# Performance work log

Hardware: AMD Instinct MI355X
Metric: run time of the kernel (lower is better)

## Reference

```python
import jax, jax.numpy as jnp
import numpy as np

B, M, H, NH = 64, 512, 1024, 8
HD = H // NH
EPS = 1e-5


def setup_inputs() -> dict:
    key = jax.random.key(0)
    ks = jax.random.split(key, 16)
    def n(k, shape, s=0.02):
        return jax.random.normal(k, shape, dtype=jnp.float32) * s
    z = lambda shape: jnp.zeros(shape, jnp.float32)
    return {
        "x": jax.random.normal(ks[0], (B, M, M), dtype=jnp.float32),
        # 1x1 Conv2d(1->H): weight [H,1,1,1] flattened to [H], plus bias [H]
        "conv_w": n(ks[1], (H,)), "conv_b": n(ks[2], (H,)),
        # MLP: Linear(M->H), ReLU, Linear(H->H); weights stored [in,out]
        "w1": n(ks[3], (M, H)), "b1": z((H,)),
        "w2": n(ks[4], (H, H)), "b2": z((H,)),
        "ln_g": jnp.ones((H,), jnp.float32), "ln_b": z((H,)),
        "wq": n(ks[5], (H, H)), "bq": z((H,)),
        "wk": n(ks[6], (H, H)), "bk": z((H,)),
        "wv": n(ks[7], (H, H)), "bv": z((H,)),
        "wo": n(ks[8], (H, H)), "bo": z((H,)),
        "wp": n(ks[9], (H, H)), "bp": z((H,)),
    }


def reference(x, conv_w, conv_b, w1, b1, w2, b2, ln_g, ln_b,
              wq, bq, wk, bk, wv, bv, wo, bo, wp, bp):
    # RegionConvolution: 1x1 conv over 1 input channel to H channels, then
    # mean over channels. Since mean_c(x*w_c + b_c) = x*mean(w) + mean(b),
    # compute the reduced affine form (identical math, no [B,H,M,M] temp).
    x = x + (x * conv_w.mean() + conv_b.mean())          # residual conv add, [B,M,M]
    # RegionEmbeddingMLP
    x_reg = jnp.maximum(x @ w1 + b1, 0.0) @ w2 + b2      # [B,M,H]
    # LayerNorm
    mu = x_reg.mean(-1, keepdims=True)
    var = ((x_reg - mu) ** 2).mean(-1, keepdims=True)
    x_norm = (x_reg - mu) / jnp.sqrt(var + EPS) * ln_g + ln_b
    # MHSA with multiplicative off-diagonal mask (diagonal scores zeroed)
    def heads(y):
        return y.reshape(B, M, NH, HD).transpose(0, 2, 1, 3)  # [B,NH,M,HD]
    q = heads(x_norm @ wq + bq)
    k = heads(x_norm @ wk + bk)
    v = heads(x_norm @ wv + bv)
    scores = jnp.einsum('bhqd,bhkd->bhqk', q, k) / jnp.sqrt(jnp.float32(HD))
    scores = scores * (1.0 - jnp.eye(M, dtype=scores.dtype))  # zero diagonal
    attn = jax.nn.softmax(scores, axis=-1)
    ctx = jnp.einsum('bhqk,bhkd->bhqd', attn, v)
    ctx = ctx.transpose(0, 2, 1, 3).reshape(B, M, H)
    attn_out = ctx @ wo + bo
    attn_out = attn_out @ wp + bp                        # output_proj
    return attn_out + x_reg                              # residual, [B,M,H]
```

## Files before the change

kernel.cpp:

```cpp
#include <hip/hip_runtime.h>
#include <hip/hip_fp16.h>
#include <cstdint>
#include <cstddef>

typedef _Float16 f16;
typedef _Float16 f16x8 __attribute__((ext_vector_type(8)));
typedef _Float16 f16x4 __attribute__((ext_vector_type(4)));
typedef _Float16 f16x2 __attribute__((ext_vector_type(2)));
typedef float f32x4 __attribute__((ext_vector_type(4)));
typedef unsigned int ui4 __attribute__((ext_vector_type(4)));

#define NB 64
#define SEQ 512
#define HDIM 1024
#define NHEAD 8
#define HD 128
#define MR (NB * SEQ)
#define QK_LD 2048

__device__ __forceinline__ void async_copy16(const f16* g, f16* l) {
  __builtin_amdgcn_global_load_lds(
      (__attribute__((address_space(1))) void*)(void*)const_cast<f16*>(g),
      (__attribute__((address_space(3))) void*)l, 16, 0, 0);
}


__global__ __launch_bounds__(256) void conv_reduce(
    const float* __restrict__ cw, const float* __restrict__ cb,
    float* __restrict__ out2) {
  int t = threadIdx.x;
  float a = 0.f, b = 0.f;
  for (int i = t; i < HDIM; i += 256) { a += cw[i]; b += cb[i]; }
  for (int m = 32; m >= 1; m >>= 1) { a += __shfl_xor(a, m); b += __shfl_xor(b, m); }
  __shared__ float sa[4], sb[4];
  if ((t & 63) == 0) { sa[t >> 6] = a; sb[t >> 6] = b; }
  __syncthreads();
  if (t == 0) {
    out2[0] = (sa[0] + sa[1] + sa[2] + sa[3]) * (1.f / HDIM);
    out2[1] = (sb[0] + sb[1] + sb[2] + sb[3]) * (1.f / HDIM);
  }
}

__global__ __launch_bounds__(256) void prep_x(
    const float* __restrict__ x, const float* __restrict__ cs,
    f16* __restrict__ xh) {
  size_t i = (size_t)blockIdx.x * 256 + threadIdx.x;
  float cw = 1.f + cs[0], cb = cs[1];
  float4 v = ((const float4*)x)[i];
  f16x4 o;
  o[0] = (f16)(v.x * cw + cb);
  o[1] = (f16)(v.y * cw + cb);
  o[2] = (f16)(v.z * cw + cb);
  o[3] = (f16)(v.w * cw + cb);
  ((f16x4*)xh)[i] = o;
}

__global__ __launch_bounds__(256) void concat_bias(
    const float* __restrict__ bq, const float* __restrict__ bk,
    const float* __restrict__ bv, float* __restrict__ dst) {
  int i = blockIdx.x * 256 + threadIdx.x;
  if (i < 1024) dst[i] = bq[i];
  else if (i < 2048) dst[i] = bk[i - 1024];
  else dst[i] = bv[i - 2048];
}

__global__ __launch_bounds__(256) void cast_f16(
    const float* __restrict__ src, f16* __restrict__ dst) {
  size_t i = (size_t)blockIdx.x * 256 + threadIdx.x;
  float4 v = ((const float4*)src)[i];
  f16x4 o;
  o[0] = (f16)v.x; o[1] = (f16)v.y; o[2] = (f16)v.z; o[3] = (f16)v.w;
  ((f16x4*)dst)[i] = o;
}

__global__ __launch_bounds__(256) void fuse_bias_p1(
    const float* __restrict__ bo, const float* __restrict__ wp,
    float* __restrict__ partial) {
  int n = blockIdx.x * 256 + threadIdx.x;
  int jc = blockIdx.y;
  float s = 0.f;
#pragma unroll 8
  for (int j = jc * 128; j < jc * 128 + 128; j++) s += bo[j] * wp[(size_t)j * 1024 + n];
  partial[(size_t)jc * 1024 + n] = s;
}

__global__ __launch_bounds__(256) void fuse_bias_p2(
    const float* __restrict__ partial, const float* __restrict__ bp,
    float* __restrict__ bp2) {
  int n = blockIdx.x * 256 + threadIdx.x;
  float s = bp[n];
#pragma unroll
  for (int jc = 0; jc < 8; jc++) s += partial[(size_t)jc * 1024 + n];
  bp2[n] = s;
}

__global__ __launch_bounds__(256) void transpose_cast(
    const float* __restrict__ src, f16* __restrict__ dst, int K, int N) {
  __shared__ float tile[32][33];
  int tx = threadIdx.x, ty = threadIdx.y;
  int n0 = blockIdx.x * 32, k0 = blockIdx.y * 32;
#pragma unroll
  for (int r = 0; r < 32; r += 8) tile[ty + r][tx] = src[(size_t)(k0 + ty + r) * N + n0 + tx];
  __syncthreads();
#pragma unroll
  for (int r = 0; r < 32; r += 8)
    dst[(size_t)(n0 + ty + r) * K + k0 + tx] = (f16)tile[tx][ty + r];
}

__global__ __launch_bounds__(256) void transpose_cast5(
    const float* s0, const float* s1, const float* s2, const float* s3, const float* s4,
    f16* d0, f16* d1, f16* d2, f16* d3, f16* d4) {
  const float* src; f16* dst;
  switch (blockIdx.z) {
    case 0: src = s0; dst = d0; break;
    case 1: src = s1; dst = d1; break;
    case 2: src = s2; dst = d2; break;
    case 3: src = s3; dst = d3; break;
    default: src = s4; dst = d4; break;
  }
  __shared__ float tile[32][33];
  int tx = threadIdx.x, ty = threadIdx.y;
  int n0 = blockIdx.x * 32, k0 = blockIdx.y * 32;
#pragma unroll
  for (int r = 0; r < 32; r += 8) tile[ty + r][tx] = src[(size_t)(k0 + ty + r) * 1024 + n0 + tx];
  __syncthreads();
#pragma unroll
  for (int r = 0; r < 32; r += 8)
    dst[(size_t)(n0 + ty + r) * 1024 + k0 + tx] = (f16)tile[tx][ty + r];
}

__global__ __launch_bounds__(256) void ln_kernel(
    const f16* __restrict__ xin, const float* __restrict__ g,
    const float* __restrict__ bta, f16* __restrict__ out) {
  int row = blockIdx.x;
  int t = threadIdx.x;
  f16x4 vh = ((const f16x4*)(xin + (size_t)row * HDIM))[t];
  float vx = (float)vh[0], vy = (float)vh[1], vz = (float)vh[2], vw = (float)vh[3];
  float s = vx + vy + vz + vw;
  float s2 = vx * vx + vy * vy + vz * vz + vw * vw;
  for (int m = 32; m >= 1; m >>= 1) { s += __shfl_xor(s, m); s2 += __shfl_xor(s2, m); }
  __shared__ float sa[4], sb[4];
  if ((t & 63) == 0) { sa[t >> 6] = s; sb[t >> 6] = s2; }
  __syncthreads();
  float S = sa[0] + sa[1] + sa[2] + sa[3];
  float S2 = sb[0] + sb[1] + sb[2] + sb[3];
  float mu = S * (1.f / HDIM);
  float var = S2 * (1.f / HDIM) - mu * mu;
  float inv = rsqrtf(var + 1e-5f);
  float4 gv = ((const float4*)g)[t];
  float4 bv = ((const float4*)bta)[t];
  f16x4 o;
  o[0] = (f16)((vx - mu) * inv * gv.x + bv.x);
  o[1] = (f16)((vy - mu) * inv * gv.y + bv.y);
  o[2] = (f16)((vz - mu) * inv * gv.z + bv.z);
  o[3] = (f16)((vw - mu) * inv * gv.w + bv.w);
  ((f16x4*)(out + (size_t)row * HDIM))[t] = o;
}

template <int EPI>
__global__ __launch_bounds__(512) void gemm_nt(
    const f16* __restrict__ A, const f16* __restrict__ BT,
    const float* __restrict__ bias, void* __restrict__ Cout, int N, int K,
    const f16* __restrict__ Xres, f16* __restrict__ vTout) {
  __shared__ __align__(16) f16 As[128 * 64];
  __shared__ __align__(16) f16 Bs[128 * 64];
  const int tid = threadIdx.x;
  const int wave = tid >> 6, lane = tid & 63;
  const int l15 = lane & 15, quad = lane >> 4;

  const int gn = N >> 7;
  const int gm = (int)gridDim.x / gn;
  const int pid = blockIdx.x;
  const int npg = 16 * gn;
  const int gid = pid / npg;
  const int rem = pid - gid * npg;
  const int grows = min(16, gm - gid * 16);
  const int bm = gid * 16 + rem % grows;
  const int bn = rem / grows;

  const int wm = wave >> 2, wn = wave & 3;

  f32x4 z4 = {0.f, 0.f, 0.f, 0.f};
  f32x4 acc[4][2];
#pragma unroll
  for (int i = 0; i < 4; i++)
#pragma unroll
    for (int j = 0; j < 2; j++) acc[i][j] = z4;

  const int srow = tid >> 3;
  const int c = ((tid & 7) - (srow & 7)) & 7;
  const f16* Ag = A + (size_t)(bm * 128 + srow) * K + c * 8;
  const f16* Bg = BT + (size_t)(bn * 128 + srow) * K + c * 8;
  f16* Al0 = As + tid * 8;
  f16* Al1 = As + 64 * 64 + tid * 8;
  f16* Bl0 = Bs + tid * 8;
  f16* Bl1 = Bs + 64 * 64 + tid * 8;
  const size_t kstep = (size_t)64 * K;

  const int r7 = l15 & 7;

  for (int k0 = 0; k0 < K; k0 += 64) {
    async_copy16(Ag, Al0);
    async_copy16(Ag + kstep, Al1);
    async_copy16(Bg, Bl0);
    async_copy16(Bg + kstep, Bl1);
    Ag += 64; Bg += 64;
    __syncthreads();
#pragma unroll
    for (int s = 0; s < 2; s++) {
      f16x8 af[4], bfr[2];
#pragma unroll
      for (int t = 0; t < 4; t++) {
        int phys = (s * 4 + quad + r7) & 7;
        af[t] = *(const f16x8*)&As[(wm * 64 + t * 16 + l15) * 64 + phys * 8];
      }
#pragma unroll
      for (int u = 0; u < 2; u++) {
        int phys = (s * 4 + quad + r7) & 7;
        bfr[u] = *(const f16x8*)&Bs[(wn * 32 + u * 16 + l15) * 64 + phys * 8];
      }
#pragma unroll
      for (int i = 0; i < 4; i++)
#pragma unroll
        for (int j = 0; j < 2; j++)
          acc[i][j] = __builtin_amdgcn_mfma_f32_16x16x32_f16(af[i], bfr[j], acc[i][j], 0, 0, 0);
    }
    __syncthreads();
  }

  float* Cf = (float*)Cout;
  f16* Ch = (f16*)Cout;
#pragma unroll
  for (int i = 0; i < 4; i++) {
    int r0 = bm * 128 + wm * 64 + i * 16 + quad * 4;
#pragma unroll
    for (int j = 0; j < 2; j++) {
      int c0 = bn * 128 + wn * 32 + j * 16;
      int cc = c0 + l15;
      float bv = (EPI == 4) ? 0.f : bias[cc];
      if (EPI == 6 && c0 >= 2048) {
        int hh = (cc - 2048) >> 7, d = (cc - 2048) & 127;
        int bb = r0 >> 9, ml = r0 & 511;
        f16x4 o;
#pragma unroll
        for (int reg = 0; reg < 4; reg++) o[reg] = (f16)(acc[i][j][reg] + bv);
        *(f16x4*)&vTout[((size_t)(bb * NHEAD + hh) * HD + d) * SEQ + ml] = o;
      } else {
#pragma unroll
        for (int reg = 0; reg < 4; reg++) {
          float v = acc[i][j][reg] + bv;
          if (EPI == 0)      Ch[(size_t)(r0 + reg) * N + cc] = (f16)fmaxf(v, 0.f);
          else if (EPI == 1) Ch[(size_t)(r0 + reg) * N + cc] = (f16)v;
          else if (EPI == 4) Ch[(size_t)(r0 + reg) * N + cc] = (f16)v;
          else if (EPI == 5) {
            size_t idx = (size_t)(r0 + reg) * N + cc;
            Cf[idx] = v + (float)Xres[idx];
          } else {
            Ch[(size_t)(r0 + reg) * QK_LD + cc] = (f16)v;
          }
        }
      }
    }
  }
}

__global__ __launch_bounds__(512) void attn_kernel(
    const f16* __restrict__ qkv, const f16* __restrict__ vT,
    f16* __restrict__ ctx) {
  const int tid = threadIdx.x;
  const int wave = tid >> 6, lane = tid & 63;
  const int l15 = lane & 15, quad = lane >> 4;
  const int bidx = blockIdx.x;
  const int qc = bidx >> 9;
  const int bh = bidx & 511;
  const int h = bh & 7, bb = bh >> 3;

  const f16* Qbase = qkv + (size_t)(bb * SEQ) * QK_LD + h * 128;
  const f16* Kbase = Qbase + 1024;
  const f16* VTbase = vT + (size_t)(bb * NHEAD + h) * HD * SEQ;

  __shared__ __align__(16) f16 Ks[64 * 128];
  __shared__ __align__(16) f16 VTs[128 * 64];

  const float scale = 0.08838834764831845f;
  const int qrow0 = qc * 256 + wave * 32;
  f16x8 qf[2][4];
#pragma unroll
  for (int tm = 0; tm < 2; tm++)
#pragma unroll
    for (int s = 0; s < 4; s++) {
      qf[tm][s] = *(const f16x8*)(Qbase + (size_t)(qrow0 + tm * 16 + l15) * QK_LD + s * 32 + quad * 8);
#pragma unroll
      for (int e = 0; e < 8; e++) qf[tm][s][e] *= (f16)scale;
    }

  f32x4 z4 = {0.f, 0.f, 0.f, 0.f};
  f32x4 O[2][8];
#pragma unroll
  for (int i = 0; i < 2; i++)
#pragma unroll
    for (int j = 0; j < 8; j++) O[i][j] = z4;
  float lrow[2] = {0.f, 0.f};

  const int kc = ((tid & 15) - ((tid >> 4) & 15)) & 15;
  const f16* Kg = Kbase + (size_t)(tid >> 4) * QK_LD + kc * 8;
  f16* Kl = Ks + tid * 8;
  const int vc = ((tid & 7) - ((tid >> 3) & 7)) & 7;
  const f16* Vg = VTbase + (size_t)(tid >> 3) * SEQ + vc * 8;
  f16* Vl = VTs + tid * 8;

  const int r7 = l15 & 7;
  const bool qodd = (quad & 1) != 0;

  for (int kt = 0; kt < 8; kt++) {
    const int krow0 = kt * 64;
#pragma unroll
    for (int i = 0; i < 2; i++)
      async_copy16(Kg + (size_t)(krow0 + 32 * i) * QK_LD, Kl + 4096 * i);
#pragma unroll
    for (int i = 0; i < 2; i++)
      async_copy16(Vg + (size_t)(64 * i) * SEQ + krow0, Vl + 4096 * i);
    __syncthreads();

    f32x4 ST[4][2];
#pragma unroll
    for (int i = 0; i < 4; i++)
#pragma unroll
      for (int j = 0; j < 2; j++) ST[i][j] = z4;
#pragma unroll
    for (int s = 0; s < 4; s++) {
      f16x8 bfr[4];
#pragma unroll
      for (int tn = 0; tn < 4; tn++) {
        int phys = (s * 4 + quad + l15) & 15;
        bfr[tn] = *(const f16x8*)&Ks[(tn * 16 + l15) * 128 + phys * 8];
      }
      __builtin_amdgcn_s_setprio(1);
#pragma unroll
      for (int tn = 0; tn < 4; tn++)
#pragma unroll
        for (int tm = 0; tm < 2; tm++)
          ST[tn][tm] = __builtin_amdgcn_mfma_f32_16x16x32_f16(bfr[tn], qf[tm][s], ST[tn][tm], 0, 0, 0);
      __builtin_amdgcn_s_setprio(0);
    }

    f16x8 pa[2][2];
#pragma unroll
    for (int tm = 0; tm < 2; tm++) {
      const int qg = qrow0 + tm * 16 + l15;
      float rs = 0.f;
      unsigned int H[4][2];
#pragma unroll
      for (int tn = 0; tn < 4; tn++) {
        float p[4];
#pragma unroll
        for (int reg = 0; reg < 4; reg++) {
          int kg = krow0 + tn * 16 + quad * 4 + reg;
          float v = (kg == qg) ? 1.f : __expf(ST[tn][tm][reg]);
          p[reg] = v;
          rs += v;
        }
        f16x2 h01 = {(f16)p[0], (f16)p[1]};
        f16x2 h23 = {(f16)p[2], (f16)p[3]};
        H[tn][0] = __builtin_bit_cast(unsigned int, h01);
        H[tn][1] = __builtin_bit_cast(unsigned int, h23);
      }
      rs += __shfl_xor(rs, 16);
      rs += __shfl_xor(rs, 32);
      lrow[tm] += rs;

#pragma unroll
      for (int ks = 0; ks < 2; ks++) {
        unsigned int a0 = H[ks * 2][0], a1 = H[ks * 2][1];
        unsigned int b0 = H[ks * 2 + 1][0], b1 = H[ks * 2 + 1][1];
        asm volatile("s_nop 1\n\tv_permlane32_swap_b32 %0, %1\n\ts_nop 1"
                     : "+v"(a0), "+v"(b0));
        asm volatile("s_nop 1\n\tv_permlane32_swap_b32 %0, %1\n\ts_nop 1"
                     : "+v"(a1), "+v"(b1));
        unsigned int c0 = (unsigned int)__shfl_xor((int)a0, 16);
        unsigned int c1 = (unsigned int)__shfl_xor((int)a1, 16);
        unsigned int d0 = (unsigned int)__shfl_xor((int)b0, 16);
        unsigned int d1 = (unsigned int)__shfl_xor((int)b1, 16);
        ui4 wv;
        wv[0] = qodd ? d0 : a0;
        wv[1] = qodd ? d1 : a1;
        wv[2] = qodd ? b0 : c0;
        wv[3] = qodd ? b1 : c1;
        pa[tm][ks] = __builtin_bit_cast(f16x8, wv);
      }
    }

#pragma unroll
    for (int ks = 0; ks < 2; ks++) {
      __builtin_amdgcn_s_setprio(1);
#pragma unroll
      for (int tn = 0; tn < 8; tn++) {
        int phys = (ks * 4 + quad + r7) & 7;
        f16x8 vb = *(const f16x8*)&VTs[(tn * 16 + l15) * 64 + phys * 8];
#pragma unroll
        for (int tm = 0; tm < 2; tm++)
          O[tm][tn] = __builtin_amdgcn_mfma_f32_16x16x32_f16(pa[tm][ks], vb, O[tm][tn], 0, 0, 0);
      }
      __builtin_amdgcn_s_setprio(0);
    }
    __syncthreads();
  }

#pragma unroll
  for (int tm = 0; tm < 2; tm++)
#pragma unroll
    for (int reg = 0; reg < 4; reg++) {
      float lv = __shfl(lrow[tm], quad * 4 + reg);
      float inv = 1.f / lv;
      int row = bb * SEQ + qrow0 + tm * 16 + quad * 4 + reg;
#pragma unroll
      for (int tn = 0; tn < 8; tn++) {
        int col = h * 128 + tn * 16 + l15;
        ctx[(size_t)row * HDIM + col] = (f16)(O[tm][tn][reg] * inv);
      }
    }
}


extern "C" void kernel_launch(void* const* d_in, const int* in_sizes, int n_in,
                              void* d_out, int out_size, void* d_ws, size_t ws_size,
                              hipStream_t stream) {
  (void)in_sizes; (void)n_in; (void)out_size; (void)ws_size;
  const float* x      = (const float*)d_in[0];
  const float* conv_w = (const float*)d_in[1];
  const float* conv_b = (const float*)d_in[2];
  const float* w1     = (const float*)d_in[3];
  const float* b1     = (const float*)d_in[4];
  const float* w2     = (const float*)d_in[5];
  const float* b2     = (const float*)d_in[6];
  const float* ln_g   = (const float*)d_in[7];
  const float* ln_b   = (const float*)d_in[8];
  const float* wq     = (const float*)d_in[9];
  const float* bq     = (const float*)d_in[10];
  const float* wk     = (const float*)d_in[11];
  const float* bk     = (const float*)d_in[12];
  const float* wv     = (const float*)d_in[13];
  const float* bv     = (const float*)d_in[14];
  const float* wo     = (const float*)d_in[15];
  const float* bo     = (const float*)d_in[16];
  const float* wp     = (const float*)d_in[17];
  const float* bp     = (const float*)d_in[18];
  float* out = (float*)d_out;

  char* ws = (char*)d_ws;
  size_t off = 0;
  auto alloc = [&](size_t bytes) {
    char* p = ws + off;
    off += (bytes + 255) & ~(size_t)255;
    return p;
  };
  float* cs    = (float*)alloc(8);
  f16* w1T     = (f16*)alloc((size_t)1024 * 512 * 2);
  f16* w2T     = (f16*)alloc((size_t)1024 * 1024 * 2);
  f16* qkvT    = (f16*)alloc((size_t)3072 * 1024 * 2);
  f16* wpT     = (f16*)alloc((size_t)1024 * 1024 * 2);
  f16* woh     = (f16*)alloc((size_t)1024 * 1024 * 2);
  f16* woPT    = (f16*)alloc((size_t)1024 * 1024 * 2);
  float* bqkv  = (float*)alloc((size_t)3072 * 4);
  float* bp2   = (float*)alloc((size_t)1024 * 4);
  float* part  = (float*)alloc((size_t)8 * 1024 * 4);
  f16* qkvQK   = (f16*)alloc((size_t)MR * QK_LD * 2);
  f16* h1      = (f16*)alloc((size_t)MR * 1024 * 2);
  f16* x_norm  = (f16*)alloc((size_t)MR * 1024 * 2);
  f16* x_regh  = (f16*)alloc((size_t)MR * 1024 * 2);
  f16* xh = qkvQK;
  f16* vT = h1;
  f16* ctx = x_norm;

  dim3 tb(32, 8);
  conv_reduce<<<1, 256, 0, stream>>>(conv_w, conv_b, cs);
  transpose_cast<<<dim3(32, 16), tb, 0, stream>>>(w1, w1T, 512, 1024);
  transpose_cast5<<<dim3(32, 32, 5), tb, 0, stream>>>(
      w2, wq, wk, wv, wp,
      w2T, qkvT, qkvT + (size_t)1024 * 1024, qkvT + (size_t)2048 * 1024, wpT);
  cast_f16<<<1024, 256, 0, stream>>>(wo, woh);
  concat_bias<<<12, 256, 0, stream>>>(bq, bk, bv, bqkv);
  fuse_bias_p1<<<dim3(4, 8), 256, 0, stream>>>(bo, wp, part);
  fuse_bias_p2<<<4, 256, 0, stream>>>(part, bp, bp2);
  prep_x<<<16384, 256, 0, stream>>>(x, cs, xh);

  gemm_nt<4><<<dim3(64), 512, 0, stream>>>(wpT, woh, nullptr, (void*)woPT, 1024, 1024, nullptr, nullptr);

  gemm_nt<0><<<dim3(256 * 8), 512, 0, stream>>>(xh, w1T, b1, (void*)h1, 1024, 512, nullptr, nullptr);
  gemm_nt<1><<<dim3(256 * 8), 512, 0, stream>>>(h1, w2T, b2, (void*)x_regh, 1024, 1024, nullptr, nullptr);
  ln_kernel<<<32768, 256, 0, stream>>>(x_regh, ln_g, ln_b, x_norm);
  gemm_nt<6><<<dim3(256 * 24), 512, 0, stream>>>(x_norm, qkvT, bqkv, (void*)qkvQK, 3072, 1024, nullptr, vT);
  attn_kernel<<<1024, 512, 0, stream>>>(qkvQK, vT, ctx);
  gemm_nt<5><<<dim3(256 * 8), 512, 0, stream>>>(ctx, woPT, bp2, (void*)out, 1024, 1024, x_regh, nullptr);
}
```

Measured before the change: 854.2 us.

## Double-buffer K/V tiles in attention kernel with async prefetch

Shared-memory K and V^T tiles are doubled, so the next tile's async global-to-LDS copies are issued before the current tile is computed. Partial vmcnt waits and raw barriers replace the full __syncthreads, overlapping load latency with the QK and PV MFMA work. This doubles LDS use per block (64KB), which may lower occupancy, and it relies on the hand-counted vmcnt values and the omitted lgkmcnt wait being correct.

New measurement: 853.9 us. Within noise of the previous version (-0.0%).

```diff
diff --git a/kernel.cpp b/kernel.cpp
--- a/kernel.cpp
+++ b/kernel.cpp
@@ -279,8 +279,8 @@
   const f16* Kbase = Qbase + 1024;
   const f16* VTbase = vT + (size_t)(bb * NHEAD + h) * HD * SEQ;
 
-  __shared__ __align__(16) f16 Ks[64 * 128];
-  __shared__ __align__(16) f16 VTs[128 * 64];
+  __shared__ __align__(16) f16 Ks[2 * 64 * 128];
+  __shared__ __align__(16) f16 VTs[2 * 128 * 64];
 
   const float scale = 0.08838834764831845f;
   const int qrow0 = qc * 256 + wave * 32;
@@ -304,23 +304,38 @@
 
   const int kc = ((tid & 15) - ((tid >> 4) & 15)) & 15;
   const f16* Kg = Kbase + (size_t)(tid >> 4) * QK_LD + kc * 8;
-  f16* Kl = Ks + tid * 8;
   const int vc = ((tid & 7) - ((tid >> 3) & 7)) & 7;
   const f16* Vg = VTbase + (size_t)(tid >> 3) * SEQ + vc * 8;
-  f16* Vl = VTs + tid * 8;
 
   const int r7 = l15 & 7;
   const bool qodd = (quad & 1) != 0;
 
+#define STAGE_KV_(BUF, KT) do {                                               \
+    const int kr_ = (KT) * 64;                                                \
+    _Pragma("unroll") for (int i_ = 0; i_ < 2; i_++)                          \
+      async_copy16(Kg + (size_t)(kr_ + 32 * i_) * QK_LD,                      \
+                   Ks + (BUF) * 8192 + tid * 8 + 4096 * i_);                  \
+    _Pragma("unroll") for (int i_ = 0; i_ < 2; i_++)                          \
+      async_copy16(Vg + (size_t)(64 * i_) * SEQ + kr_,                        \
+                   VTs + (BUF) * 8192 + tid * 8 + 4096 * i_);                 \
+  } while (0)
+
+  asm volatile("s_waitcnt vmcnt(0)" ::: "memory");
+  STAGE_KV_(0, 0);
+
   for (int kt = 0; kt < 8; kt++) {
+    const int buf = kt & 1;
+    const f16* Ksb = Ks + buf * 8192;
+    const f16* VTsb = VTs + buf * 8192;
     const int krow0 = kt * 64;
-#pragma unroll
-    for (int i = 0; i < 2; i++)
-      async_copy16(Kg + (size_t)(krow0 + 32 * i) * QK_LD, Kl + 4096 * i);
-#pragma unroll
-    for (int i = 0; i < 2; i++)
-      async_copy16(Vg + (size_t)(64 * i) * SEQ + krow0, Vl + 4096 * i);
-    __syncthreads();
+
+    if (kt < 7) {
+      STAGE_KV_(buf ^ 1, kt + 1);
+      asm volatile("s_waitcnt vmcnt(4)" ::: "memory");
+    } else {
+      asm volatile("s_waitcnt vmcnt(0)" ::: "memory");
+    }
+    __builtin_amdgcn_s_barrier();
 
     f32x4 ST[4][2];
 #pragma unroll
@@ -333,7 +348,7 @@
 #pragma unroll
       for (int tn = 0; tn < 4; tn++) {
         int phys = (s * 4 + quad + l15) & 15;
-        bfr[tn] = *(const f16x8*)&Ks[(tn * 16 + l15) * 128 + phys * 8];
+        bfr[tn] = *(const f16x8*)&Ksb[(tn * 16 + l15) * 128 + phys * 8];
       }
       __builtin_amdgcn_s_setprio(1);
 #pragma unroll
@@ -396,15 +411,16 @@
 #pragma unroll
       for (int tn = 0; tn < 8; tn++) {
         int phys = (ks * 4 + quad + r7) & 7;
-        f16x8 vb = *(const f16x8*)&VTs[(tn * 16 + l15) * 64 + phys * 8];
+        f16x8 vb = *(const f16x8*)&VTsb[(tn * 16 + l15) * 64 + phys * 8];
 #pragma unroll
         for (int tm = 0; tm < 2; tm++)
           O[tm][tn] = __builtin_amdgcn_mfma_f32_16x16x32_f16(pa[tm][ks], vb, O[tm][tn], 0, 0, 0);
       }
       __builtin_amdgcn_s_setprio(0);
     }
-    __syncthreads();
+    __builtin_amdgcn_s_barrier();
   }
+#undef STAGE_KV_
 
 #pragma unroll
   for (int tm = 0; tm < 2; tm++)
```
